# Performance work log

Measured on AMD Instinct MI355X. Metric: run time of the kernel, lower is better.

The kernel has to match this reference:

```python
import jax, jax.numpy as jnp
import numpy as np

WIDTH = 64          # grid size -> seq_len = WIDTH*WIDTH = 4096
EMBED = 128
BATCH = 8


def setup_inputs() -> dict:
    key = jax.random.key(0)
    ks = jax.random.split(key, 12)
    B, S, E = BATCH, WIDTH * WIDTH, EMBED
    scale = 1.0 / np.sqrt(E)
    inp = {
        "queries": jax.random.normal(ks[0], (B, S, E), jnp.float32),
        "keys": jax.random.normal(ks[1], (B, S, E), jnp.float32),
        "values": jax.random.normal(ks[2], (B, S, E), jnp.float32),
        # oracle_edges: [B, num_paths, num_edges, 2(endpoints), 2(x,y)] with coords in [0, WIDTH)
        "oracle_edges": jax.random.randint(ks[3], (B, 32, 16, 2, 2), 0, WIDTH, jnp.int32),
        "Wq": jax.random.uniform(ks[4], (E, E), jnp.float32, -scale, scale),
        "bq": jax.random.uniform(ks[5], (E,), jnp.float32, -scale, scale),
        "Wk": jax.random.uniform(ks[6], (E, E), jnp.float32, -scale, scale),
        "bk": jax.random.uniform(ks[7], (E,), jnp.float32, -scale, scale),
        "Wv": jax.random.uniform(ks[8], (E, E), jnp.float32, -scale, scale),
        "bv": jax.random.uniform(ks[9], (E,), jnp.float32, -scale, scale),
        "Wp": jax.random.uniform(ks[10], (E, E), jnp.float32, -scale, scale),
        "bp": jax.random.uniform(ks[11], (E,), jnp.float32, -scale, scale),
    }
    return inp


def reference(queries, keys, values, oracle_edges, Wq, bq, Wk, bk, Wv, bv, Wp, bp):
    B, S, E = queries.shape
    # Q/K projections are computed by the original module but never used
    # (the 'attention' is just the oracle adjacency) -- dead code, omitted.
    v = values @ Wv + bv                              # [B,S,E]

    # Build dense 0/1 adjacency from edge lists: node = y*WIDTH + x
    e = oracle_edges.reshape(B, -1, 2, 2)             # [B, P*E, 2, 2]
    nodes = e[..., 1] * WIDTH + e[..., 0]             # [B, P*E, 2]
    src, dst = nodes[..., 0], nodes[..., 1]
    b_idx = jnp.arange(B)[:, None]
    A = jnp.zeros((B, S, S), jnp.float32).at[b_idx, src, dst].set(1.0)

    hidden = jnp.einsum("bst,btd->bsd", A, v)         # [B,S,E]
    attn_repr = hidden @ Wp + bp                      # [B,S,E]

    # num_heads == 1: mean over head dim is identity; residual=False so
    # mask == adjacency == A.
    return attn_repr, A, A
```

## Files before the change

kernel.cpp:

```cpp
#include <hip/hip_runtime.h>

#define WIDTH 64
#define S 4096
#define E 128
#define BATCH 8
#define EDGES_PER_B 512
#define TOTAL_EDGES (BATCH * EDGES_PER_B)

typedef float vfloat4 __attribute__((ext_vector_type(4)));

__global__ void init_attn_kernel(float* __restrict__ attn,
                                 const float* __restrict__ bp) {
    const int i = blockIdx.x * blockDim.x + threadIdx.x;
    const int e0 = (i * 4) & (E - 1);
    vfloat4 v = {bp[e0], bp[e0 + 1], bp[e0 + 2], bp[e0 + 3]};
    __builtin_nontemporal_store(v, reinterpret_cast<vfloat4*>(attn) + i);
}

__global__ void dedupe_kernel(const int* __restrict__ edges,
                              int* __restrict__ flags) {
    const int b = blockIdx.x;
    __shared__ int keys[EDGES_PER_B];
    const int4* eb = reinterpret_cast<const int4*>(edges) + b * EDGES_PER_B;
    for (int i = threadIdx.x; i < EDGES_PER_B; i += blockDim.x) {
        int4 e = eb[i];
        int src = e.y * WIDTH + e.x;
        int dst = e.w * WIDTH + e.z;
        keys[i] = src * S + dst;
    }
    __syncthreads();
    for (int i = threadIdx.x; i < EDGES_PER_B; i += blockDim.x) {
        int k = keys[i];
        int uniq = 1;
        for (int j = 0; j < i; ++j) {
            if (keys[j] == k) { uniq = 0; break; }
        }
        flags[b * EDGES_PER_B + i] = uniq;
    }
}

__global__ void scatter_kernel(const int* __restrict__ edges,
                               const int* __restrict__ flags,
                               const float* __restrict__ values,
                               const float* __restrict__ Wv,
                               const float* __restrict__ bv,
                               const float* __restrict__ Wp,
                               float* __restrict__ attn,
                               float* __restrict__ A1,
                               float* __restrict__ A2) {
    const int g = blockIdx.x;
    const int b = g >> 9;
    int4 e = reinterpret_cast<const int4*>(edges)[g];
    const int src = e.y * WIDTH + e.x;
    const int dst = e.w * WIDTH + e.z;
    const int aidx = (b * S + src) * S + dst;
    if (threadIdx.x == 0) A1[aidx] = 1.0f;
    if (threadIdx.x == 1) A2[aidx] = 1.0f;
    if (!flags[g]) return;

    __shared__ float sv[E];
    __shared__ float hv[E];
    const int t = threadIdx.x;
    sv[t] = values[(b * S + dst) * E + t];
    __syncthreads();
    float acc = bv[t];
#pragma unroll 8
    for (int k = 0; k < E; ++k) acc += sv[k] * Wv[k * E + t];
    hv[t] = acc;
    __syncthreads();
    float p = 0.0f;
#pragma unroll 8
    for (int k = 0; k < E; ++k) p += hv[k] * Wp[k * E + t];
    atomicAdd(&attn[(b * S + src) * E + t], p);
}

extern "C" void kernel_launch(void* const* d_in, const int* in_sizes, int n_in,
                              void* d_out, int out_size, void* d_ws,
                              size_t ws_size, hipStream_t stream) {
    const float* values = (const float*)d_in[2];
    const int*   edges  = (const int*)d_in[3];
    const float* Wv     = (const float*)d_in[8];
    const float* bv     = (const float*)d_in[9];
    const float* Wp     = (const float*)d_in[10];
    const float* bp     = (const float*)d_in[11];

    float* out  = (float*)d_out;
    float* attn = out;
    float* A1   = out + (size_t)BATCH * S * E;
    float* A2   = A1 + (size_t)BATCH * S * S;

    int* flags = (int*)d_ws;

    (void)hipMemsetAsync(A1, 0, (size_t)2 * BATCH * S * S * sizeof(float),
                         stream);

    init_attn_kernel<<<4096, 256, 0, stream>>>(attn, bp);

    dedupe_kernel<<<BATCH, 256, 0, stream>>>(edges, flags);
    scatter_kernel<<<TOTAL_EDGES, 128, 0, stream>>>(edges, flags, values, Wv,
                                                    bv, Wp, attn, A1, A2);
}
```

Baseline: 1.150 ms.

## Replace atomic per-edge scatter with per-source gather using linearity of projections

```diff
diff --git a/kernel.cpp b/kernel.cpp
--- a/kernel.cpp
+++ b/kernel.cpp
@@ -7,36 +7,131 @@
 #define EDGES_PER_B 512
 #define TOTAL_EDGES (BATCH * EDGES_PER_B)
 
+#define ATTN_FLOATS (BATCH * S * E)
+#define ATTN_N4 (ATTN_FLOATS / 4)
+
+#define GATHER_BLOCKS 256
+#define SLOTS (TOTAL_EDGES / GATHER_BLOCKS)
+
 typedef float vfloat4 __attribute__((ext_vector_type(4)));
 
-__global__ void init_attn_kernel(float* __restrict__ attn,
-                                 const float* __restrict__ bp) {
-    const int i = blockIdx.x * blockDim.x + threadIdx.x;
-    const int e0 = (i * 4) & (E - 1);
-    vfloat4 v = {bp[e0], bp[e0 + 1], bp[e0 + 2], bp[e0 + 3]};
-    __builtin_nontemporal_store(v, reinterpret_cast<vfloat4*>(attn) + i);
+__global__ __launch_bounds__(256) void init_attn_kernel(
+    float* __restrict__ attn, const float* __restrict__ bp) {
+    const int i = blockIdx.x * 256 + threadIdx.x;
+    reinterpret_cast<vfloat4*>(attn)[i] =
+        reinterpret_cast<const vfloat4*>(bp)[i & (E / 4 - 1)];
 }
 
 __global__ void dedupe_kernel(const int* __restrict__ edges,
-                              int* __restrict__ flags) {
+                              int* __restrict__ pairflag,
+                              int* __restrict__ leader) {
     const int b = blockIdx.x;
     __shared__ int keys[EDGES_PER_B];
+    __shared__ int srcs[EDGES_PER_B];
     const int4* eb = reinterpret_cast<const int4*>(edges) + b * EDGES_PER_B;
     for (int i = threadIdx.x; i < EDGES_PER_B; i += blockDim.x) {
         int4 e = eb[i];
         int src = e.y * WIDTH + e.x;
         int dst = e.w * WIDTH + e.z;
+        srcs[i] = src;
         keys[i] = src * S + dst;
     }
     __syncthreads();
     for (int i = threadIdx.x; i < EDGES_PER_B; i += blockDim.x) {
-        int k = keys[i];
-        int uniq = 1;
+        int k = keys[i], s = srcs[i];
+        int uq = 1, ld = 1;
         for (int j = 0; j < i; ++j) {
-            if (keys[j] == k) { uniq = 0; break; }
+            if (keys[j] == k) uq = 0;
+            if (srcs[j] == s) ld = 0;
         }
-        flags[b * EDGES_PER_B + i] = uniq;
-    }
+        pairflag[b * EDGES_PER_B + i] = uq;
+        leader[b * EDGES_PER_B + i] = ld;
+    }
+}
+
+__global__ __launch_bounds__(128) void gather_kernel(
+    const int* __restrict__ edges, const int* __restrict__ pairflag,
+    const int* __restrict__ leader, const float* __restrict__ values,
+    const float* __restrict__ Wv, const float* __restrict__ bv,
+    const float* __restrict__ Wp, const float* __restrict__ bp,
+    float* __restrict__ attn) {
+    __shared__ float Wl[E * E];
+    __shared__ float hv_all[SLOTS][E];
+    __shared__ float vsum[E];
+    __shared__ float bvs[E];
+    __shared__ float bps[E];
+    __shared__ int s_src[EDGES_PER_B];
+    __shared__ int s_dst[EDGES_PER_B];
+    __shared__ int s_flag[EDGES_PER_B];
+    __shared__ int slot_src[SLOTS];
+
+    const int t = threadIdx.x;
+    const int blk = blockIdx.x;
+    const int b = blk / (GATHER_BLOCKS / BATCH);
+    const int e0 = blk * SLOTS;
+    const int ib0 = e0 & (EDGES_PER_B - 1);
+
+    const int4* eb = reinterpret_cast<const int4*>(edges) + b * EDGES_PER_B;
+    for (int i = t; i < EDGES_PER_B; i += 128) {
+        int4 e = eb[i];
+        s_src[i] = e.y * WIDTH + e.x;
+        s_dst[i] = e.w * WIDTH + e.z;
+        s_flag[i] = pairflag[b * EDGES_PER_B + i];
+    }
+    bvs[t] = bv[t];
+    bps[t] = bp[t];
+    for (int i = t; i < E * E / 4; i += 128)
+        reinterpret_cast<vfloat4*>(Wl)[i] =
+            reinterpret_cast<const vfloat4*>(Wv)[i];
+    __syncthreads();
+
+    for (int s = 0; s < SLOTS; ++s) {
+        const int gi = e0 + s;
+        if (t == 0) slot_src[s] = -1;
+        if (!leader[gi]) continue;
+        const int src = s_src[ib0 + s];
+        if (t == 0) slot_src[s] = src;
+        float vs = 0.0f, fcnt = 0.0f;
+        for (int j = 0; j < EDGES_PER_B; ++j) {
+            if (s_src[j] == src && s_flag[j]) {
+                vs += values[((size_t)(b * S + s_dst[j])) * E + t];
+                fcnt += 1.0f;
+            }
+        }
+        vsum[t] = vs;
+        __syncthreads();
+        float acc = fcnt * bvs[t];
+#pragma unroll 8
+        for (int k = 0; k < E; ++k) acc += vsum[k] * Wl[k * E + t];
+        hv_all[s][t] = acc;
+        __syncthreads();
+    }
+    __syncthreads();
+
+    for (int i = t; i < E * E / 4; i += 128)
+        reinterpret_cast<vfloat4*>(Wl)[i] =
+            reinterpret_cast<const vfloat4*>(Wp)[i];
+    __syncthreads();
+
+    for (int s = 0; s < SLOTS; ++s) {
+        const int src = slot_src[s];
+        if (src < 0) continue;
+        float p = bps[t];
+#pragma unroll 8
+        for (int k = 0; k < E; ++k) p += hv_all[s][k] * Wl[k * E + t];
+        attn[((size_t)(b * S + src)) * E + t] = p;
+    }
+}
+
+__global__ __launch_bounds__(256) void ones_kernel(
+    const int* __restrict__ edges, float* __restrict__ A1,
+    float* __restrict__ A2) {
+    const int g = blockIdx.x * 256 + threadIdx.x;
+    int4 e = reinterpret_cast<const int4*>(edges)[g];
+    const int b = g >> 9;
+    const int aidx = (b * S + e.y * WIDTH + e.x) * S + (e.w * WIDTH + e.z);
+    A1[aidx] = 1.0f;
+    A2[aidx] = 1.0f;
 }
 
 __global__ void scatter_kernel(const int* __restrict__ edges,
@@ -57,7 +152,6 @@
     if (threadIdx.x == 0) A1[aidx] = 1.0f;
     if (threadIdx.x == 1) A2[aidx] = 1.0f;
     if (!flags[g]) return;
-
     __shared__ float sv[E];
     __shared__ float hv[E];
     const int t = threadIdx.x;
@@ -72,6 +166,24 @@
 #pragma unroll 8
     for (int k = 0; k < E; ++k) p += hv[k] * Wp[k * E + t];
     atomicAdd(&attn[(b * S + src) * E + t], p);
+}
+
+__global__ void dedupe_only_kernel(const int* __restrict__ edges,
+                                   int* __restrict__ flags) {
+    const int b = blockIdx.x;
+    __shared__ int keys[EDGES_PER_B];
+    const int4* eb = reinterpret_cast<const int4*>(edges) + b * EDGES_PER_B;
+    for (int i = threadIdx.x; i < EDGES_PER_B; i += blockDim.x) {
+        int4 e = eb[i];
+        keys[i] = (e.y * WIDTH + e.x) * S + (e.w * WIDTH + e.z);
+    }
+    __syncthreads();
+    for (int i = threadIdx.x; i < EDGES_PER_B; i += blockDim.x) {
+        int k = keys[i], uq = 1;
+        for (int j = 0; j < i; ++j)
+            if (keys[j] == k) { uq = 0; break; }
+        flags[b * EDGES_PER_B + i] = uq;
+    }
 }
 
 extern "C" void kernel_launch(void* const* d_in, const int* in_sizes, int n_in,
@@ -89,14 +201,22 @@
     float* A1   = out + (size_t)BATCH * S * E;
     float* A2   = A1 + (size_t)BATCH * S * S;
 
-    int* flags = (int*)d_ws;
-
     (void)hipMemsetAsync(A1, 0, (size_t)2 * BATCH * S * S * sizeof(float),
                          stream);
 
-    init_attn_kernel<<<4096, 256, 0, stream>>>(attn, bp);
-
-    dedupe_kernel<<<BATCH, 256, 0, stream>>>(edges, flags);
-    scatter_kernel<<<TOTAL_EDGES, 128, 0, stream>>>(edges, flags, values, Wv,
-                                                    bv, Wp, attn, A1, A2);
-}
+    init_attn_kernel<<<ATTN_N4 / 256, 256, 0, stream>>>(attn, bp);
+
+    if (ws_size >= (size_t)2 * TOTAL_EDGES * sizeof(int)) {
+        int* pairflag = (int*)d_ws;
+        int* leader   = pairflag + TOTAL_EDGES;
+        dedupe_kernel<<<BATCH, 256, 0, stream>>>(edges, pairflag, leader);
+        gather_kernel<<<GATHER_BLOCKS, 128, 0, stream>>>(
+            edges, pairflag, leader, values, Wv, bv, Wp, bp, attn);
+        ones_kernel<<<TOTAL_EDGES / 256, 256, 0, stream>>>(edges, A1, A2);
+    } else {
+        int* flags = (int*)d_ws;
+        dedupe_only_kernel<<<BATCH, 256, 0, stream>>>(edges, flags);
+        scatter_kernel<<<TOTAL_EDGES, 128, 0, stream>>>(
+            edges, flags, values, Wv, bv, Wp, attn, A1, A2);
+    }
+}
```

Measured after the change: 1.561 ms. 1.36x slower.

## Group edges by source row, sum values before projecting, drop dedupe kernel

Applied to the files above, without the earlier changes.

```diff
diff --git a/kernel.cpp b/kernel.cpp
--- a/kernel.cpp
+++ b/kernel.cpp
@@ -7,71 +7,93 @@
 #define EDGES_PER_B 512
 #define TOTAL_EDGES (BATCH * EDGES_PER_B)
 
+#define ATTN_FLOATS (BATCH * S * E)
+#define ATTN_N4 (ATTN_FLOATS / 4)
+
 typedef float vfloat4 __attribute__((ext_vector_type(4)));
 
-__global__ void init_attn_kernel(float* __restrict__ attn,
-                                 const float* __restrict__ bp) {
-    const int i = blockIdx.x * blockDim.x + threadIdx.x;
-    const int e0 = (i * 4) & (E - 1);
-    vfloat4 v = {bp[e0], bp[e0 + 1], bp[e0 + 2], bp[e0 + 3]};
-    __builtin_nontemporal_store(v, reinterpret_cast<vfloat4*>(attn) + i);
+
+__global__ __launch_bounds__(256) void init_attn_kernel(
+    float* __restrict__ attn, const float* __restrict__ bp) {
+    const int i = blockIdx.x * 256 + threadIdx.x;
+    reinterpret_cast<vfloat4*>(attn)[i] =
+        reinterpret_cast<const vfloat4*>(bp)[i & (E / 4 - 1)];
 }
 
-__global__ void dedupe_kernel(const int* __restrict__ edges,
-                              int* __restrict__ flags) {
-    const int b = blockIdx.x;
-    __shared__ int keys[EDGES_PER_B];
-    const int4* eb = reinterpret_cast<const int4*>(edges) + b * EDGES_PER_B;
-    for (int i = threadIdx.x; i < EDGES_PER_B; i += blockDim.x) {
-        int4 e = eb[i];
-        int src = e.y * WIDTH + e.x;
-        int dst = e.w * WIDTH + e.z;
-        keys[i] = src * S + dst;
-    }
-    __syncthreads();
-    for (int i = threadIdx.x; i < EDGES_PER_B; i += blockDim.x) {
-        int k = keys[i];
-        int uniq = 1;
-        for (int j = 0; j < i; ++j) {
-            if (keys[j] == k) { uniq = 0; break; }
-        }
-        flags[b * EDGES_PER_B + i] = uniq;
-    }
-}
-
-__global__ void scatter_kernel(const int* __restrict__ edges,
-                               const int* __restrict__ flags,
-                               const float* __restrict__ values,
-                               const float* __restrict__ Wv,
-                               const float* __restrict__ bv,
-                               const float* __restrict__ Wp,
-                               float* __restrict__ attn,
-                               float* __restrict__ A1,
-                               float* __restrict__ A2) {
+__global__ __launch_bounds__(128) void scatter3_kernel(
+    const int* __restrict__ edges, const float* __restrict__ values,
+    const float* __restrict__ Wv, const float* __restrict__ bv,
+    const float* __restrict__ Wp, const float* __restrict__ bp,
+    float* __restrict__ attn, float* __restrict__ A1,
+    float* __restrict__ A2) {
     const int g = blockIdx.x;
     const int b = g >> 9;
-    int4 e = reinterpret_cast<const int4*>(edges)[g];
+    const int ib = g & (EDGES_PER_B - 1);
+    const int4 e = reinterpret_cast<const int4*>(edges)[g];
     const int src = e.y * WIDTH + e.x;
     const int dst = e.w * WIDTH + e.z;
     const int aidx = (b * S + src) * S + dst;
     if (threadIdx.x == 0) A1[aidx] = 1.0f;
     if (threadIdx.x == 1) A2[aidx] = 1.0f;
-    if (!flags[g]) return;
 
-    __shared__ float sv[E];
+    __shared__ int s_src[EDGES_PER_B];
+    __shared__ int s_dst[EDGES_PER_B];
+    __shared__ int gidx[EDGES_PER_B];
+    __shared__ int nl;
+    __shared__ int gcnt;
+    __shared__ float vsum[E];
     __shared__ float hv[E];
     const int t = threadIdx.x;
-    sv[t] = values[(b * S + dst) * E + t];
+    if (t == 0) { nl = 0; gcnt = 0; }
+    const int4* eb = reinterpret_cast<const int4*>(edges) + b * EDGES_PER_B;
+#pragma unroll
+    for (int r = 0; r < EDGES_PER_B / 128; ++r) {
+        const int i = t + r * 128;
+        int4 ee = eb[i];
+        s_src[i] = ee.y * WIDTH + ee.x;
+        s_dst[i] = ee.w * WIDTH + ee.z;
+    }
     __syncthreads();
-    float acc = bv[t];
+
+#pragma unroll
+    for (int r = 0; r < EDGES_PER_B / 128; ++r) {
+        const int j = t + r * 128;
+        if (s_src[j] == src) {
+            if (j < ib) nl = 1;
+            gidx[atomicAdd(&gcnt, 1)] = j;
+        }
+    }
+    __syncthreads();
+    if (nl) return;
+
+    const int gsz = gcnt;
+    float vs = 0.0f, fcnt = 0.0f;
+    for (int m = 0; m < gsz; ++m) {
+        const int jm = gidx[m];
+        const int dm = s_dst[jm];
+        bool uq = true;
+        for (int mm = 0; mm < gsz; ++mm) {
+            const int jmm = gidx[mm];
+            if (jmm < jm && s_dst[jmm] == dm) uq = false;
+        }
+        if (uq) {
+            vs += values[(size_t)(b * S + dm) * E + t];
+            fcnt += 1.0f;
+        }
+    }
+    vsum[t] = vs;
+    __syncthreads();
+
+    float acc = fcnt * bv[t];
 #pragma unroll 8
-    for (int k = 0; k < E; ++k) acc += sv[k] * Wv[k * E + t];
+    for (int k = 0; k < E; ++k) acc += vsum[k] * Wv[k * E + t];
     hv[t] = acc;
     __syncthreads();
-    float p = 0.0f;
+
+    float p = bp[t];
 #pragma unroll 8
     for (int k = 0; k < E; ++k) p += hv[k] * Wp[k * E + t];
-    atomicAdd(&attn[(b * S + src) * E + t], p);
+    attn[(size_t)(b * S + src) * E + t] = p;
 }
 
 extern "C" void kernel_launch(void* const* d_in, const int* in_sizes, int n_in,
@@ -89,14 +111,11 @@
     float* A1   = out + (size_t)BATCH * S * E;
     float* A2   = A1 + (size_t)BATCH * S * S;
 
-    int* flags = (int*)d_ws;
-
     (void)hipMemsetAsync(A1, 0, (size_t)2 * BATCH * S * S * sizeof(float),
                          stream);
 
-    init_attn_kernel<<<4096, 256, 0, stream>>>(attn, bp);
+    init_attn_kernel<<<ATTN_N4 / 256, 256, 0, stream>>>(attn, bp);
 
-    dedupe_kernel<<<BATCH, 256, 0, stream>>>(edges, flags);
-    scatter_kernel<<<TOTAL_EDGES, 128, 0, stream>>>(edges, flags, values, Wv,
-                                                    bv, Wp, attn, A1, A2);
+    scatter3_kernel<<<TOTAL_EDGES, 128, 0, stream>>>(
+        edges, values, Wv, bv, Wp, bp, attn, A1, A2);
 }
```

After: 1.082 ms. 1.06x faster.
